# Kernel optimization log

Hardware: AMD Instinct MI355X
Metric: run time of the kernel (lower is better)

## Reference

```python
import jax, jax.numpy as jnp
import numpy as np

B, S, D, H = 4, 2048, 1024, 16
HD = D // H


def setup_inputs() -> dict:
    key = jax.random.key(0)
    ks = jax.random.split(key, 9)
    s = 1.0 / np.sqrt(D)
    return {
        "x": jax.random.normal(ks[0], (B, S, D), dtype=jnp.float32),
        "wq": jax.random.uniform(ks[1], (D, D), jnp.float32, -s, s),
        "bq": jax.random.uniform(ks[2], (D,), jnp.float32, -s, s),
        "wk": jax.random.uniform(ks[3], (D, D), jnp.float32, -s, s),
        "bk": jax.random.uniform(ks[4], (D,), jnp.float32, -s, s),
        "wv": jax.random.uniform(ks[5], (D, D), jnp.float32, -s, s),
        "bv": jax.random.uniform(ks[6], (D,), jnp.float32, -s, s),
        "wo": jax.random.uniform(ks[7], (D, D), jnp.float32, -s, s),
        "bo": jax.random.uniform(ks[8], (D,), jnp.float32, -s, s),
    }


def reference(x, wq, bq, wk, bk, wv, bv, wo, bo):
    b, s, _ = x.shape
    # QKV projections, split into heads: [B, H, S, HD]
    q = (x @ wq + bq).reshape(b, s, H, HD).transpose(0, 2, 1, 3)
    k = (x @ wk + bk).reshape(b, s, H, HD).transpose(0, 2, 1, 3)
    v = (x @ wv + bv).reshape(b, s, H, HD).transpose(0, 2, 1, 3)
    # Full score matrix [B, H, S, S] as the original does
    scores = jnp.einsum("bhqd,bhkd->bhqk", q, k) / jnp.sqrt(jnp.float32(HD))
    attn = jax.nn.softmax(scores, axis=-1)  # dropout is identity in eval mode
    ctx = jnp.einsum("bhqk,bhkd->bhqd", attn, v)
    ctx = ctx.transpose(0, 2, 1, 3).reshape(b, s, D)
    return ctx @ wo + bo
```

## Files before the change

### kernel.cpp

```cpp
#include <hip/hip_runtime.h>
#include <hip/hip_bf16.h>
#include <stdint.h>

#define B_  4
#define S_  2048
#define D_  1024
#define H_  16
#define HD_ 64

using bf16x8 = __attribute__((ext_vector_type(8))) short;
using f32x4  = __attribute__((ext_vector_type(4))) float;
using f32x16 = __attribute__((ext_vector_type(16))) float;
using i32x2  = __attribute__((ext_vector_type(2))) int;
using i32x4  = __attribute__((ext_vector_type(4))) int;

#define QSCALE 0.18033688011112042f

#if __has_builtin(__builtin_amdgcn_exp2f)
#define EXP2F(x) __builtin_amdgcn_exp2f(x)
#else
#define EXP2F(x) exp2f(x)
#endif

__device__ __forceinline__ short f2b(float f) {
  union { __hip_bfloat16 h; short s; } u;
  u.h = __float2bfloat16(f);
  return u.s;
}

__device__ __forceinline__ unsigned cvtpk(float lo, float hi) {
  unsigned r;
  asm("v_cvt_pk_bf16_f32 %0, %1, %2" : "=v"(r) : "v"(lo), "v"(hi));
  return r;
}

__device__ __forceinline__ void g2lds16(const void* g, void* l) {
  __builtin_amdgcn_global_load_lds(
      (const __attribute__((address_space(1))) uint32_t*)(uintptr_t)g,
      (__attribute__((address_space(3))) uint32_t*)(uint32_t)(uintptr_t)l,
      16, 0, 0);
}


__global__ __launch_bounds__(256) void k_cvt_x(const float* __restrict__ x,
                                               short* __restrict__ xb, int n8) {
  int i = blockIdx.x * 256 + threadIdx.x;
  if (i >= n8) return;
  const float4* xp = (const float4*)x;
  float4 a = xp[2 * i], b = xp[2 * i + 1];
  bf16x8 o;
  o[0] = f2b(a.x); o[1] = f2b(a.y); o[2] = f2b(a.z); o[3] = f2b(a.w);
  o[4] = f2b(b.x); o[5] = f2b(b.y); o[6] = f2b(b.z); o[7] = f2b(b.w);
  ((bf16x8*)xb)[i] = o;
}

__global__ __launch_bounds__(256) void k_cvt_w(
    const float* __restrict__ wq, const float* __restrict__ wk,
    const float* __restrict__ wv, const float* __restrict__ wo,
    short* __restrict__ wqkvT, short* __restrict__ woT) {
  __shared__ float tile[32][33];
  int wi = blockIdx.z;
  const float* src = wi == 0 ? wq : wi == 1 ? wk : wi == 2 ? wv : wo;
  float scale = (wi == 0) ? QSCALE : 1.0f;
  short* dst = wi < 3 ? wqkvT + (size_t)wi * D_ * D_ : woT;
  int n0 = blockIdx.x * 32, k0 = blockIdx.y * 32;
  int tx = threadIdx.x, ty = threadIdx.y;
#pragma unroll
  for (int j = 0; j < 4; ++j)
    tile[ty + j * 8][tx] = src[(size_t)(k0 + ty + j * 8) * D_ + n0 + tx];
  __syncthreads();
#pragma unroll
  for (int j = 0; j < 4; ++j)
    dst[(size_t)(n0 + ty + j * 8) * D_ + k0 + tx] = f2b(tile[tx][ty + j * 8] * scale);
}

__global__ void k_cvt_b(const float* __restrict__ bq, const float* __restrict__ bk,
                        const float* __restrict__ bv, float* __restrict__ biasqkv) {
  int i = blockIdx.x * 256 + threadIdx.x;
  if (i >= 3 * D_) return;
  float v = (i < D_) ? bq[i] * QSCALE : (i < 2 * D_) ? bk[i - D_] : bv[i - 2 * D_];
  biasqkv[i] = v;
}


template <int MODE>
__global__ __launch_bounds__(256, 2) void k_gemm(
    const short* __restrict__ A, const short* __restrict__ Bt,
    const float* __restrict__ bias, float* __restrict__ outF,
    short* __restrict__ Qo, short* __restrict__ Ko, short* __restrict__ Vo) {
  constexpr int K = 1024;
  __shared__ short Als[128 * 64];
  __shared__ short Bls[128 * 64];
  const int tid = threadIdx.x;
  const int wave = tid >> 6, lane = tid & 63;
  const int wr = wave >> 1, wc = wave & 1;
  const int l15 = lane & 15, l4 = lane >> 4;
  const int rowBase = blockIdx.x * 128;
  const int colBase = blockIdx.y * 128;

  f32x4 zero4 = {0.f, 0.f, 0.f, 0.f};
  f32x4 acc[4][4];
#pragma unroll
  for (int m = 0; m < 4; ++m)
#pragma unroll
    for (int n = 0; n < 4; ++n) acc[m][n] = zero4;

  for (int kt = 0; kt < K; kt += 64) {
#pragma unroll
    for (int i = 0; i < 4; ++i) {
      int c = i * 256 + tid;
      int r = c >> 3;
      int ko = ((c & 7) * 8) ^ ((r & 7) << 3);
      g2lds16(A + (size_t)(rowBase + r) * K + kt + ko, &Als[(i * 256 + wave * 64) * 8]);
      g2lds16(Bt + (size_t)(colBase + r) * K + kt + ko, &Bls[(i * 256 + wave * 64) * 8]);
    }
    __syncthreads();
#pragma unroll
    for (int kk = 0; kk < 2; ++kk) {
      bf16x8 af[4], bfr[4];
#pragma unroll
      for (int m = 0; m < 4; ++m) {
        int r = wr * 64 + m * 16 + l15;
        af[m] = *(const bf16x8*)&Als[r * 64 + ((kk * 32 + l4 * 8) ^ ((r & 7) << 3))];
      }
#pragma unroll
      for (int n = 0; n < 4; ++n) {
        int r = wc * 64 + n * 16 + l15;
        bfr[n] = *(const bf16x8*)&Bls[r * 64 + ((kk * 32 + l4 * 8) ^ ((r & 7) << 3))];
      }
#pragma unroll
      for (int m = 0; m < 4; ++m)
#pragma unroll
        for (int n = 0; n < 4; ++n)
          acc[m][n] = __builtin_amdgcn_mfma_f32_16x16x32_bf16(af[m], bfr[n], acc[m][n], 0, 0, 0);
    }
    __syncthreads();
  }

#pragma unroll
  for (int n = 0; n < 4; ++n) {
    int n_g = colBase + wc * 64 + n * 16 + l15;
    float bia = bias[n_g];
#pragma unroll
    for (int m = 0; m < 4; ++m) {
#pragma unroll
      for (int r = 0; r < 4; ++r) {
        int m_g = rowBase + wr * 64 + m * 16 + l4 * 4 + r;
        float v = acc[m][n][r] + bia;
        if constexpr (MODE == 0) {
          int p = n_g >> 10, dm = n_g & 1023, h = dm >> 6, hd = dm & 63;
          int b = m_g >> 11, s = m_g & 2047;
          short* dst = p == 0 ? Qo : p == 1 ? Ko : Vo;
          size_t idx;
          if (p == 2) idx = ((size_t)((b * H_ + h) * HD_ + hd)) * S_ + s;
          else        idx = ((size_t)((b * H_ + h) * S_ + s)) * HD_ + hd;
          dst[idx] = f2b(v);
        } else {
          outF[(size_t)m_g * D_ + n_g] = v;
        }
      }
    }
  }
}


__global__ __launch_bounds__(256, 3) void k_attn2(
    const short* __restrict__ Q, const short* __restrict__ K,
    const short* __restrict__ Vt, short* __restrict__ ctx) {
  __shared__ short Kls[2][64 * 64];
  __shared__ short Vls[2][64 * 64];
  const int bh = blockIdx.y;
  const int q0 = blockIdx.x * 128;
  const int tid = threadIdx.x, wave = tid >> 6, lane = tid & 63;
  const int l31 = lane & 31, hi = lane >> 5;
  const short* Qb = Q + (size_t)bh * S_ * HD_;
  const short* Kb = K + (size_t)bh * S_ * HD_;
  const short* Vb = Vt + (size_t)bh * HD_ * S_;

  bf16x8 qf[4];
#pragma unroll
  for (int ks = 0; ks < 4; ++ks)
    qf[ks] = *(const bf16x8*)&Qb[(size_t)(q0 + wave * 32 + l31) * HD_ + ks * 16 + hi * 8];

  f32x16 ctxa[2];
#pragma unroll
  for (int n = 0; n < 2; ++n)
#pragma unroll
    for (int i = 0; i < 16; ++i) ctxa[n][i] = 0.f;
  float m = -1e30f, lsum = 0.f;

#define STAGE(kv0, b)                                                          \
  {                                                                            \
    _Pragma("unroll") for (int i = 0; i < 2; ++i) {                            \
      int c = i * 256 + tid;                                                   \
      int r = c >> 3;                                                          \
      int off = ((c & 7) * 8) ^ ((r & 7) << 3);                                \
      g2lds16(Kb + (size_t)((kv0) + r) * HD_ + off,                            \
              &Kls[b][(i * 256 + wave * 64) * 8]);                             \
      g2lds16(Vb + (size_t)r * S_ + (kv0) + off,                               \
              &Vls[b][(i * 256 + wave * 64) * 8]);                             \
    }                                                                          \
  }

  STAGE(0, 0);
  int buf = 0;
#pragma unroll 1
  for (int t = 0; t < S_ / 64; ++t) {
    __syncthreads();
    STAGE((((t + 1) & 31) * 64), (buf ^ 1));

    f32x16 sa[2];
#pragma unroll
    for (int tt = 0; tt < 2; ++tt) {
#pragma unroll
      for (int i = 0; i < 16; ++i) sa[tt][i] = 0.f;
#pragma unroll
      for (int ks = 0; ks < 4; ++ks) {
        int r = tt * 32 + l31;
        bf16x8 kf = *(const bf16x8*)&Kls[buf][r * 64 + ((ks * 16 + hi * 8) ^ ((r & 7) << 3))];
        sa[tt] = __builtin_amdgcn_mfma_f32_32x32x16_bf16(kf, qf[ks], sa[tt], 0, 0, 0);
      }
    }

    float red[16];
#pragma unroll
    for (int i = 0; i < 16; ++i) red[i] = fmaxf(sa[0][i], sa[1][i]);
#pragma unroll
    for (int st = 8; st > 0; st >>= 1)
#pragma unroll
      for (int i = 0; i < st; ++i) red[i] = fmaxf(red[i], red[i + st]);
    float mx = fmaxf(red[0], __shfl_xor(red[0], 32));
    float mnew = fmaxf(m, mx);
    float corr = EXP2F(m - mnew);
#pragma unroll
    for (int tt = 0; tt < 2; ++tt)
#pragma unroll
      for (int i = 0; i < 16; ++i) sa[tt][i] = EXP2F(sa[tt][i] - mnew);
#pragma unroll
    for (int i = 0; i < 16; ++i) red[i] = sa[0][i] + sa[1][i];
#pragma unroll
    for (int st = 8; st > 0; st >>= 1)
#pragma unroll
      for (int i = 0; i < st; ++i) red[i] += red[i + st];
    float rs = red[0] + __shfl_xor(red[0], 32);
    lsum = lsum * corr + rs;
    m = mnew;
#pragma unroll
    for (int n = 0; n < 2; ++n)
#pragma unroll
      for (int i = 0; i < 16; ++i) ctxa[n][i] *= corr;

#pragma unroll
    for (int ks = 0; ks < 4; ++ks) {
      int tt = ks >> 1, s1 = ks & 1;
      unsigned x0 = cvtpk(sa[tt][8 * s1 + 0], sa[tt][8 * s1 + 1]);
      unsigned x1 = cvtpk(sa[tt][8 * s1 + 2], sa[tt][8 * s1 + 3]);
      unsigned y0 = cvtpk(sa[tt][8 * s1 + 4], sa[tt][8 * s1 + 5]);
      unsigned y1 = cvtpk(sa[tt][8 * s1 + 6], sa[tt][8 * s1 + 7]);
      i32x2 r0 = __builtin_amdgcn_permlane32_swap((int)x0, (int)y0, false, false);
      i32x2 r1 = __builtin_amdgcn_permlane32_swap((int)x1, (int)y1, false, false);
      union { i32x4 i; bf16x8 h; } pu;
      pu.i = (i32x4){r0[0], r1[0], r0[1], r1[1]};
#pragma unroll
      for (int nn = 0; nn < 2; ++nn) {
        int r = nn * 32 + l31;
        bf16x8 vf = *(const bf16x8*)&Vls[buf][r * 64 + ((ks * 16 + hi * 8) ^ ((r & 7) << 3))];
        ctxa[nn] = __builtin_amdgcn_mfma_f32_32x32x16_bf16(vf, pu.h, ctxa[nn], 0, 0, 0);
      }
    }
    buf ^= 1;
  }

  __syncthreads();
  short* Pw = &Kls[0][0] + wave * 2048;
  float inv = 1.0f / lsum;
#pragma unroll
  for (int tt = 0; tt < 2; ++tt)
#pragma unroll
    for (int g = 0; g < 4; ++g) {
      unsigned d0 = cvtpk(ctxa[tt][4 * g + 0] * inv, ctxa[tt][4 * g + 1] * inv);
      unsigned d1 = cvtpk(ctxa[tt][4 * g + 2] * inv, ctxa[tt][4 * g + 3] * inv);
      int hd0 = tt * 32 + g * 8 + hi * 4;
      *(i32x2*)((char*)Pw + l31 * 128 + ((hd0 * 2) ^ ((l31 & 7) << 3))) =
          (i32x2){(int)d0, (int)d1};
    }
  __syncthreads();
  const int b = bh >> 4, h = bh & 15;
#pragma unroll
  for (int p = 0; p < 8; ++p) {
    int c = p * 64 + lane;
    int q = c >> 4, s8 = c & 15;
    i32x2 v = *(const i32x2*)((const char*)Pw + q * 128 + ((s8 * 8) ^ ((q & 7) << 3)));
    int row = q0 + wave * 32 + q;
    *(i32x2*)&ctx[((size_t)(b * S_ + row)) * D_ + h * HD_ + s8 * 4] = v;
  }
}


extern "C" void kernel_launch(void* const* d_in, const int* in_sizes, int n_in,
                              void* d_out, int out_size, void* d_ws, size_t ws_size,
                              hipStream_t stream) {
  const float* x  = (const float*)d_in[0];
  const float* wq = (const float*)d_in[1];
  const float* bq = (const float*)d_in[2];
  const float* wk = (const float*)d_in[3];
  const float* bk = (const float*)d_in[4];
  const float* wv = (const float*)d_in[5];
  const float* bv = (const float*)d_in[6];
  const float* wo = (const float*)d_in[7];
  const float* bo = (const float*)d_in[8];
  float* out = (float*)d_out;

  char* ws = (char*)d_ws;
  short* xb    = (short*)(ws);
  short* wqkvT = (short*)(ws + (16 << 20));
  short* woT   = (short*)(ws + (22 << 20));
  float* biasq = (float*)(ws + (24 << 20));
  short* Qb    = (short*)(ws + (25 << 20));
  short* Kb    = (short*)(ws + (41 << 20));
  short* Vb    = (short*)(ws + (57 << 20));

  k_cvt_x<<<dim3(4096), dim3(256), 0, stream>>>(x, xb, (B_ * S_ * D_) / 8);
  k_cvt_w<<<dim3(32, 32, 4), dim3(32, 8), 0, stream>>>(wq, wk, wv, wo, wqkvT, woT);
  k_cvt_b<<<dim3(12), dim3(256), 0, stream>>>(bq, bk, bv, biasq);

  k_gemm<0><<<dim3(64, 24), dim3(256), 0, stream>>>(xb, wqkvT, biasq,
                                                    (float*)nullptr, Qb, Kb, Vb);
  k_attn2<<<dim3(S_ / 128, B_ * H_), dim3(256), 0, stream>>>(Qb, Kb, Vb, xb );
  k_gemm<1><<<dim3(64, 8), dim3(256), 0, stream>>>(xb, woT, bo, out,
                                                   nullptr, nullptr, nullptr);
}
```

Baseline: 210.2 us.

## Lazy softmax rescale, max3 reductions, setprio around MFMA, raise attention occupancy

The attention inner loop now skips the running-max rescale of the accumulators unless some lane's new max exceeds the old one by more than 8 (log2 domain), so the correction multiply and exp run only rarely. The row-max reduction uses v_max3_f32 and the row-sum uses a vector tree reduction. s_setprio is raised around the MFMA blocks so matrix work from different waves interleaves with softmax ALU work. Launch bounds go from 3 to 4 blocks per CU, which tightens the register budget and risks spills. The lazy rescale allows exp values up to 2^8 before normalization, which is safe in fp32 but could add a little bf16 rounding error in P.

```diff
diff --git a/kernel.cpp b/kernel.cpp
--- a/kernel.cpp
+++ b/kernel.cpp
@@ -9,7 +9,9 @@
 #define HD_ 64
 
 using bf16x8 = __attribute__((ext_vector_type(8))) short;
+using f32x2  = __attribute__((ext_vector_type(2))) float;
 using f32x4  = __attribute__((ext_vector_type(4))) float;
+using f32x8  = __attribute__((ext_vector_type(8))) float;
 using f32x16 = __attribute__((ext_vector_type(16))) float;
 using i32x2  = __attribute__((ext_vector_type(2))) int;
 using i32x4  = __attribute__((ext_vector_type(4))) int;
@@ -32,6 +34,12 @@
   unsigned r;
   asm("v_cvt_pk_bf16_f32 %0, %1, %2" : "=v"(r) : "v"(lo), "v"(hi));
   return r;
+}
+
+__device__ __forceinline__ float max3f(float a, float b, float c) {
+  float d;
+  asm("v_max3_f32 %0, %1, %2, %3" : "=v"(d) : "v"(a), "v"(b), "v"(c));
+  return d;
 }
 
 __device__ __forceinline__ void g2lds16(const void* g, void* l) {
@@ -164,7 +172,7 @@
 }
 
 
-__global__ __launch_bounds__(256, 3) void k_attn2(
+__global__ __launch_bounds__(256, 4) void k_attn2(
     const short* __restrict__ Q, const short* __restrict__ K,
     const short* __restrict__ Vt, short* __restrict__ ctx) {
   __shared__ short Kls[2][64 * 64];
@@ -210,6 +218,7 @@
     STAGE((((t + 1) & 31) * 64), (buf ^ 1));
 
     f32x16 sa[2];
+    __builtin_amdgcn_s_setprio(1);
 #pragma unroll
     for (int tt = 0; tt < 2; ++tt) {
 #pragma unroll
@@ -221,35 +230,45 @@
         sa[tt] = __builtin_amdgcn_mfma_f32_32x32x16_bf16(kf, qf[ks], sa[tt], 0, 0, 0);
       }
     }
-
-    float red[16];
-#pragma unroll
-    for (int i = 0; i < 16; ++i) red[i] = fmaxf(sa[0][i], sa[1][i]);
-#pragma unroll
-    for (int st = 8; st > 0; st >>= 1)
-#pragma unroll
-      for (int i = 0; i < st; ++i) red[i] = fmaxf(red[i], red[i + st]);
-    float mx = fmaxf(red[0], __shfl_xor(red[0], 32));
-    float mnew = fmaxf(m, mx);
-    float corr = EXP2F(m - mnew);
-#pragma unroll
-    for (int tt = 0; tt < 2; ++tt)
-#pragma unroll
-      for (int i = 0; i < 16; ++i) sa[tt][i] = EXP2F(sa[tt][i] - mnew);
-#pragma unroll
-    for (int i = 0; i < 16; ++i) red[i] = sa[0][i] + sa[1][i];
-#pragma unroll
-    for (int st = 8; st > 0; st >>= 1)
-#pragma unroll
-      for (int i = 0; i < st; ++i) red[i] += red[i + st];
-    float rs = red[0] + __shfl_xor(red[0], 32);
-    lsum = lsum * corr + rs;
-    m = mnew;
-#pragma unroll
-    for (int n = 0; n < 2; ++n)
-#pragma unroll
-      for (int i = 0; i < 16; ++i) ctxa[n][i] *= corr;
-
+    __builtin_amdgcn_s_setprio(0);
+
+    float t0[8], t1[4];
+#pragma unroll
+    for (int i = 0; i < 8; ++i) t0[i] = max3f(sa[0][i], sa[0][i + 8], sa[1][i]);
+#pragma unroll
+    for (int i = 0; i < 4; ++i) t1[i] = max3f(t0[i], t0[i + 4], sa[1][i + 8]);
+    float u0 = max3f(t1[0], t1[2], sa[1][12]);
+    float u1 = max3f(t1[1], t1[3], sa[1][13]);
+    float z = max3f(u0, u1, sa[1][14]);
+    z = fmaxf(z, sa[1][15]);
+    float mx = fmaxf(z, __shfl_xor(z, 32));
+
+    if (!__all(mx - m <= 8.f)) {
+      float mnew = fmaxf(m, mx);
+      float corr = EXP2F(m - mnew);
+      lsum *= corr;
+      ctxa[0] *= corr;
+      ctxa[1] *= corr;
+      m = mnew;
+    }
+#pragma unroll
+    for (int tt = 0; tt < 2; ++tt) {
+      f32x16 dd = sa[tt] - m;
+#pragma unroll
+      for (int i = 0; i < 16; ++i) sa[tt][i] = EXP2F(dd[i]);
+    }
+    f32x16 vs = sa[0] + sa[1];
+    f32x8 a8 = __builtin_shufflevector(vs, vs, 0, 1, 2, 3, 4, 5, 6, 7)
+             + __builtin_shufflevector(vs, vs, 8, 9, 10, 11, 12, 13, 14, 15);
+    f32x4 a4 = __builtin_shufflevector(a8, a8, 0, 1, 2, 3)
+             + __builtin_shufflevector(a8, a8, 4, 5, 6, 7);
+    f32x2 a2 = __builtin_shufflevector(a4, a4, 0, 1)
+             + __builtin_shufflevector(a4, a4, 2, 3);
+    float rs = a2[0] + a2[1];
+    rs += __shfl_xor(rs, 32);
+    lsum += rs;
+
+    __builtin_amdgcn_s_setprio(1);
 #pragma unroll
     for (int ks = 0; ks < 4; ++ks) {
       int tt = ks >> 1, s1 = ks & 1;
@@ -268,6 +287,7 @@
         ctxa[nn] = __builtin_amdgcn_mfma_f32_32x32x16_bf16(vf, pu.h, ctxa[nn], 0, 0, 0);
       }
     }
+    __builtin_amdgcn_s_setprio(0);
     buf ^= 1;
   }
 
```

Result: faster. 197.2 us (-6.2%).
